# Kernel tuning notes

Measured on AMD Instinct MI355X. Metric: run time of the kernel, lower is better.

Reference implementation:

```python
import jax, jax.numpy as jnp
import numpy as np

N_NODES = 50000
N_EDGES = 500000
NUM_RADIAL = 6
HIDDEN = 128

def swish(v):
    return v * jax.nn.sigmoid(v)

def setup_inputs() -> dict:
    key = jax.random.key(0)
    ks = jax.random.split(key, 8)
    x = jax.random.randint(ks[0], (N_NODES,), 0, 95, dtype=jnp.int32)
    rbf = jax.random.normal(ks[1], (N_EDGES, NUM_RADIAL), dtype=jnp.float32)
    i = jax.random.randint(ks[2], (N_EDGES,), 0, N_NODES, dtype=jnp.int32)
    j = jax.random.randint(ks[3], (N_EDGES,), 0, N_NODES, dtype=jnp.int32)
    sqrt3 = np.sqrt(3.0).astype(np.float32)
    emb_weight = jax.random.uniform(ks[4], (95, HIDDEN), minval=-sqrt3, maxval=sqrt3, dtype=jnp.float32)
    w_rbf0 = jax.random.normal(ks[5], (HIDDEN, NUM_RADIAL), dtype=jnp.float32) * 0.2
    b_rbf0 = jnp.zeros((HIDDEN,), dtype=jnp.float32)
    w_lin = jax.random.normal(ks[6], (HIDDEN, 3 * HIDDEN), dtype=jnpp.float32) if False else jax.random.normal(ks[6], (HIDDEN, 3 * HIDDEN), dtype=jnp.float32) * 0.05
    b_lin = jnp.zeros((HIDDEN,), dtype=jnp.float32)
    w_rbf1 = jax.random.normal(ks[7], (HIDDEN, NUM_RADIAL), dtype=jnp.float32) * 0.4
    return {"x": x, "rbf": rbf, "i": i, "j": j, "emb_weight": emb_weight,
            "w_rbf0": w_rbf0, "b_rbf0": b_rbf0, "w_lin": w_lin, "b_lin": b_lin,
            "w_rbf1": w_rbf1}

def reference(x, rbf, i, j, emb_weight, w_rbf0, b_rbf0, w_lin, b_lin, w_rbf1):
    # node embedding lookup: [N, H]
    h = emb_weight[x]
    # rbf0 = swish(rbf @ W0^T + b0): [E, H]
    rbf0 = swish(jnp.einsum('er,hr->eh', rbf, w_rbf0) + b_rbf0)
    # gather endpoint embeddings and concat with rbf0: [E, 3H]
    cat = jnp.concatenate([h[i], h[j], rbf0], axis=-1)
    e1 = swish(jnp.einsum('ek,hk->eh', cat, w_lin) + b_lin)
    e2 = jnp.einsum('er,hr->eh', rbf, w_rbf1) * e1
    return (e1, e2)
```

## Files before the change

kernel.cpp:

```cpp
#include <hip/hip_runtime.h>

#define HIDDEN 128
#define NRAD 6
#define NEMB 95
#define PRS 68
#define FRS 132
#define SRS 36

typedef short bf16x8 __attribute__((ext_vector_type(8)));
typedef float f32x4 __attribute__((ext_vector_type(4)));

__device__ __forceinline__ float fast_rcp(float x) { return __builtin_amdgcn_rcpf(x); }
__device__ __forceinline__ float swishf(float v) { return v * fast_rcp(1.0f + __expf(-v)); }
__device__ __forceinline__ short f2bf(float f) {
    union { float f; unsigned u; } c; c.f = f;
    unsigned r = (c.u + 0x7FFFu + ((c.u >> 16) & 1u)) >> 16;
    return (short)(unsigned short)r;
}
__device__ __forceinline__ float bf2f(unsigned short u) {
    union { unsigned u; float f; } c; c.u = ((unsigned)u) << 16; return c.f;
}
__device__ __forceinline__ unsigned pk(float lo, float hi) {
    return __builtin_amdgcn_perm(__float_as_uint(hi), __float_as_uint(lo), 0x07060302u);
}
__device__ __forceinline__ float xlo(unsigned u) {
    union { unsigned u; float f; } c; c.u = u << 16; return c.f;
}
__device__ __forceinline__ float xhi(unsigned u) {
    union { unsigned u; float f; } c; c.u = u & 0xffff0000u; return c.f;
}
__device__ __forceinline__ void barrier_lgkm() {
    asm volatile("s_waitcnt lgkmcnt(0)" ::: "memory");
    __builtin_amdgcn_s_barrier();
}
__device__ __forceinline__ void wait_lgkm() {
    asm volatile("s_waitcnt lgkmcnt(0)" ::: "memory");
}

__global__ void precompute_kernel(const float* __restrict__ emb,
                                  const float* __restrict__ w_lin,
                                  const float* __restrict__ b_lin,
                                  unsigned* __restrict__ pPair) {
    __shared__ __align__(16) float erow[HIDDEN];
    const int a = blockIdx.x;
    const int h = threadIdx.x;
    erow[h] = emb[a * HIDDEN + h];
    __syncthreads();
    float a1 = b_lin[h];
    float a2 = 0.f;
    const float* __restrict__ w1 = w_lin + h * 384;
    const float* __restrict__ w2 = w1 + HIDDEN;
#pragma unroll 8
    for (int k = 0; k < HIDDEN; ++k) {
        a1 += erow[k] * w1[k];
        a2 += erow[k] * w2[k];
    }
    const unsigned lo = (unsigned)(unsigned short)f2bf(a1);
    const unsigned hi = ((unsigned)(unsigned short)f2bf(a2)) << 16;
    pPair[a * HIDDEN + h] = hi | lo;
}

struct RawMD {
    float2 ra, rb, rc;
    int ii, jj;
};

__device__ __forceinline__ RawMD load_raw(int st, int l15, int n_edges,
                                          const int* __restrict__ iv,
                                          const int* __restrict__ jv,
                                          const float* __restrict__ rbf) {
    int e = st * 16 + l15;
    int ecl = (e < n_edges) ? e : (n_edges - 1);
    RawMD m;
    const float2* rp = reinterpret_cast<const float2*>(rbf + (size_t)ecl * NRAD);
    m.ra = rp[0];
    m.rb = rp[1];
    m.rc = rp[2];
    m.ii = iv[ecl];
    m.jj = jv[ecl];
    return m;
}

__global__ __launch_bounds__(256, 3)
void edge_mfma_kernel(const int* __restrict__ xv,
                      const float* __restrict__ rbf,
                      const int* __restrict__ iv,
                      const int* __restrict__ jv,
                      const float* __restrict__ w_rbf0,
                      const float* __restrict__ b_rbf0,
                      const float* __restrict__ w_rbf1,
                      const float* __restrict__ w_lin,
                      const unsigned* __restrict__ pPairG,
                      float* __restrict__ out_e1,
                      float* __restrict__ out_e2,
                      int n_edges, int tiles_per_block, int nt32, int n_rows) {
    __shared__ unsigned pps[NEMB * PRS];
    __shared__ __align__(16) short fragS[2][16 * FRS];
    __shared__ __align__(8) unsigned short stg[4][2][16 * SRS];

    const int tid = threadIdx.x;
    const int chh = blockIdx.x & 1;
    const int ebi = blockIdx.x >> 1;

    {
        const int nr = (n_rows < NEMB ? n_rows : NEMB);
        for (int s = tid; s < nr * 64; s += 256) {
            const int a = s >> 6, c = s & 63;
            pps[a * PRS + c] = pPairG[a * HIDDEN + chh * 64 + c];
        }
    }

    const int wid = tid >> 6;
    const int lane = tid & 63;
    const int l15 = lane & 15;
    const int lg = lane >> 4;
    const int u = wid >> 1;
    const int c2 = wid & 1;
    const int chbase = chh * 64 + c2 * 32;

    bf16x8 w3f[2][4];
    bf16x8 w1f[2];
#pragma unroll
    for (int n2 = 0; n2 < 2; ++n2) {
        const int h = chbase + n2 * 16 + l15;
        const float* wp = w_lin + h * 384 + 256;
#pragma unroll
        for (int ks = 0; ks < 4; ++ks) {
            const float4* s4 = reinterpret_cast<const float4*>(wp + (ks * 4 + lg) * 8);
            const float4 va = s4[0];
            const float4 vb = s4[1];
            bf16x8 fr;
            fr[0] = f2bf(va.x); fr[1] = f2bf(va.y);
            fr[2] = f2bf(va.z); fr[3] = f2bf(va.w);
            fr[4] = f2bf(vb.x); fr[5] = f2bf(vb.y);
            fr[6] = f2bf(vb.z); fr[7] = f2bf(vb.w);
            w3f[n2][ks] = fr;
        }
        bf16x8 f1;
#pragma unroll
        for (int r = 0; r < NRAD; ++r) f1[r] = f2bf(w_rbf1[h * NRAD + r]);
        f1[6] = 0; f1[7] = 0;
        w1f[n2] = f1;
    }

    bf16x8 aw0[2];
#pragma unroll
    for (int i = 0; i < 2; ++i) {
        bf16x8 fr = (bf16x8){0, 0, 0, 0, 0, 0, 0, 0};
        if (lg == 0) {
            const int k = (2 * wid + i) * 16 + l15;
#pragma unroll
            for (int r = 0; r < NRAD; ++r) fr[r] = f2bf(w_rbf0[k * NRAD + r]);
            fr[6] = f2bf(b_rbf0[k]);
            fr[7] = 0;
        }
        aw0[i] = fr;
    }
    __syncthreads();

    const int bt = ebi * tiles_per_block;
    const int btEnd = min(bt + tiles_per_block, nt32);
    if (bt >= btEnd) return;

    const f32x4 zero4 = (f32x4){0.f, 0.f, 0.f, 0.f};

    RawMD c0 = load_raw(2 * bt,     l15, n_edges, iv, jv, rbf);
    RawMD c1 = load_raw(2 * bt + 1, l15, n_edges, iv, jv, rbf);

    for (int t = bt; t < btEnd; ++t) {
        RawMD n0 = load_raw(2 * (t + 1),     l15, n_edges, iv, jv, rbf);
        RawMD n1 = load_raw(2 * (t + 1) + 1, l15, n_edges, iv, jv, rbf);
        const int exi = xv[u ? c1.ii : c0.ii];
        const int exj = xv[u ? c1.jj : c0.jj];

        union { uint4 q; bf16x8 b; } rp0, rp1;
        rp0.q = (uint4){0u, 0u, 0u, 0u};
        rp1.q = (uint4){0u, 0u, 0u, 0u};
        if (lg == 0) {
            rp0.q.x = pk(c0.ra.x, c0.ra.y);
            rp0.q.y = pk(c0.rb.x, c0.rb.y);
            rp0.q.z = pk(c0.rc.x, c0.rc.y);
            rp0.q.w = pk(1.0f, 0.0f);
            rp1.q.x = pk(c1.ra.x, c1.ra.y);
            rp1.q.y = pk(c1.rb.x, c1.rb.y);
            rp1.q.z = pk(c1.rc.x, c1.rc.y);
            rp1.q.w = pk(1.0f, 0.0f);
        }

#pragma unroll
        for (int s = 0; s < 2; ++s) {
#pragma unroll
            for (int i = 0; i < 2; ++i) {
                const f32x4 cb = __builtin_amdgcn_mfma_f32_16x16x32_bf16(
                    aw0[i], (s ? rp1.b : rp0.b), zero4, 0, 0, 0);
                const uint2 wv = make_uint2(pk(swishf(cb[0]), swishf(cb[1])),
                                            pk(swishf(cb[2]), swishf(cb[3])));
                *reinterpret_cast<uint2*>(
                    &fragS[s][l15 * FRS + (4 * (2 * wid + i) + lg) * 4]) = wv;
            }
        }

        f32x4 acc2[2];
#pragma unroll
        for (int n2 = 0; n2 < 2; ++n2)
            acc2[n2] = __builtin_amdgcn_mfma_f32_16x16x32_bf16(
                w1f[n2], (u ? rp1.b : rp0.b), zero4, 0, 0, 0);

        barrier_lgkm();

        f32x4 acc[2] = {zero4, zero4};
#pragma unroll
        for (int ks = 0; ks < 4; ++ks) {
            const bf16x8 bf = *reinterpret_cast<const bf16x8*>(
                &fragS[u][l15 * FRS + (8 * ks + 2 * lg) * 4]);
#pragma unroll
            for (int n2 = 0; n2 < 2; ++n2)
                acc[n2] = __builtin_amdgcn_mfma_f32_16x16x32_bf16(
                    w3f[n2][ks], bf, acc[n2], 0, 0, 0);
        }

        barrier_lgkm();

        if (t != bt) {
            const int tp = t - 1;
#pragma unroll
            for (int arr = 0; arr < 2; ++arr) {
                float* __restrict__ ob = arr ? out_e2 : out_e1;
#pragma unroll
                for (int s = 0; s < 2; ++s) {
                    const int e = 8 * s + (lane >> 3);
                    const uint2 uv = *reinterpret_cast<const uint2*>(
                        &stg[wid][arr][e * SRS + (lane & 7) * 4]);
                    const int eg = tp * 32 + u * 16 + e;
                    if (eg < n_edges) {
                        f32x4 v;
                        v[0] = xlo(uv.x); v[1] = xhi(uv.x);
                        v[2] = xlo(uv.y); v[3] = xhi(uv.y);
                        *reinterpret_cast<f32x4*>(
                            ob + (size_t)eg * HIDDEN + chbase + (lane & 7) * 4) = v;
                    }
                }
            }
        }
        wait_lgkm();

#pragma unroll
        for (int n2 = 0; n2 < 2; ++n2) {
            const int ch0 = c2 * 32 + n2 * 16 + lg * 4;
            const uint4 r1 = *reinterpret_cast<const uint4*>(&pps[exi * PRS + ch0]);
            const uint4 r2 = *reinterpret_cast<const uint4*>(&pps[exj * PRS + ch0]);
            float pv[4];
            pv[0] = bf2f((unsigned short)(r1.x & 0xffff)) + bf2f((unsigned short)(r2.x >> 16));
            pv[1] = bf2f((unsigned short)(r1.y & 0xffff)) + bf2f((unsigned short)(r2.y >> 16));
            pv[2] = bf2f((unsigned short)(r1.z & 0xffff)) + bf2f((unsigned short)(r2.z >> 16));
            pv[3] = bf2f((unsigned short)(r1.w & 0xffff)) + bf2f((unsigned short)(r2.w >> 16));
            float e1v[4], e2v[4];
#pragma unroll
            for (int q = 0; q < 4; ++q) {
                const float sm = acc[n2][q] + pv[q];
                e1v[q] = swishf(sm);
                e2v[q] = acc2[n2][q] * e1v[q];
            }
            const int so = l15 * SRS + n2 * 16 + lg * 4;
            *reinterpret_cast<uint2*>(&stg[wid][0][so]) =
                make_uint2(pk(e1v[0], e1v[1]), pk(e1v[2], e1v[3]));
            *reinterpret_cast<uint2*>(&stg[wid][1][so]) =
                make_uint2(pk(e2v[0], e2v[1]), pk(e2v[2], e2v[3]));
        }

        c0 = n0; c1 = n1;
    }

    wait_lgkm();
    {
        const int tp = btEnd - 1;
#pragma unroll
        for (int arr = 0; arr < 2; ++arr) {
            float* __restrict__ ob = arr ? out_e2 : out_e1;
#pragma unroll
            for (int s = 0; s < 2; ++s) {
                const int e = 8 * s + (lane >> 3);
                const uint2 uv = *reinterpret_cast<const uint2*>(
                    &stg[wid][arr][e * SRS + (lane & 7) * 4]);
                const int eg = tp * 32 + u * 16 + e;
                if (eg < n_edges) {
                    f32x4 v;
                    v[0] = xlo(uv.x); v[1] = xhi(uv.x);
                    v[2] = xlo(uv.y); v[3] = xhi(uv.y);
                    *reinterpret_cast<f32x4*>(
                        ob + (size_t)eg * HIDDEN + chbase + (lane & 7) * 4) = v;
                }
            }
        }
    }
}

extern "C" void kernel_launch(void* const* d_in, const int* in_sizes, int n_in,
                              void* d_out, int out_size, void* d_ws, size_t ws_size,
                              hipStream_t stream) {
    const int*   xv     = (const int*)  d_in[0];
    const float* rbf    = (const float*)d_in[1];
    const int*   iv     = (const int*)  d_in[2];
    const int*   jv     = (const int*)  d_in[3];
    const float* emb    = (const float*)d_in[4];
    const float* w_rbf0 = (const float*)d_in[5];
    const float* b_rbf0 = (const float*)d_in[6];
    const float* w_lin  = (const float*)d_in[7];
    const float* b_lin  = (const float*)d_in[8];
    const float* w_rbf1 = (const float*)d_in[9];

    const int n_edges = in_sizes[2];
    const int n_emb_rows = in_sizes[4] / HIDDEN;

    unsigned* pPair = (unsigned*)d_ws;

    float* out_e1 = (float*)d_out;
    float* out_e2 = out_e1 + (size_t)n_edges * HIDDEN;

    precompute_kernel<<<n_emb_rows, HIDDEN, 0, stream>>>(emb, w_lin, b_lin, pPair);

    const int nt32 = (n_edges + 31) / 32;
    const int grid = 768;
    const int nEB = grid / 2;
    const int tpb = (nt32 + nEB - 1) / nEB;
    edge_mfma_kernel<<<grid, 256, 0, stream>>>(xv, rbf, iv, jv,
                                               w_rbf0, b_rbf0, w_rbf1, w_lin,
                                               pPair, out_e1, out_e2,
                                               n_edges, tpb, nt32, n_emb_rows);
}
```

Measured before the change: 176.2 us.

## Restructure edge kernel so each wave owns full 16-edge tiles independently

Replaces the block-cooperative scheme (two blocks splitting channels, four waves sharing a 32-edge tile through barriers) with one where each of 12 waves per 768-thread block processes a whole 16-edge tile across all 128 channels on its own, striding through tiles in a grid-stride loop. The w_lin third-slice weights move from registers to LDS as bf16 and are read per MFMA. The rbf0 swish is now computed with scalar FMAs per lane instead of a small MFMA. Per-iteration block barriers go away, and the per-block edge tile of the pair table no longer has to be loaded twice. The costs are much more LDS traffic for weight fragments, larger register use (16 accumulators), and fewer resident blocks per CU.

```diff
diff --git a/kernel.cpp b/kernel.cpp
--- a/kernel.cpp
+++ b/kernel.cpp
@@ -3,9 +3,11 @@
 #define HIDDEN 128
 #define NRAD 6
 #define NEMB 95
-#define PRS 68
-#define FRS 132
-#define SRS 36
+#define PRS 132
+#define WRS 132
+#define SRS 132
+#define NWAVES 12
+#define NBLK 256
 
 typedef short bf16x8 __attribute__((ext_vector_type(8)));
 typedef float f32x4 __attribute__((ext_vector_type(4)));
@@ -28,10 +30,6 @@
 }
 __device__ __forceinline__ float xhi(unsigned u) {
     union { unsigned u; float f; } c; c.u = u & 0xffff0000u; return c.f;
-}
-__device__ __forceinline__ void barrier_lgkm() {
-    asm volatile("s_waitcnt lgkmcnt(0)" ::: "memory");
-    __builtin_amdgcn_s_barrier();
 }
 __device__ __forceinline__ void wait_lgkm() {
     asm volatile("s_waitcnt lgkmcnt(0)" ::: "memory");
@@ -65,11 +63,11 @@
     int ii, jj;
 };
 
-__device__ __forceinline__ RawMD load_raw(int st, int l15, int n_edges,
+__device__ __forceinline__ RawMD load_raw(int tile, int l15, int n_edges,
                                           const int* __restrict__ iv,
                                           const int* __restrict__ jv,
                                           const float* __restrict__ rbf) {
-    int e = st * 16 + l15;
+    int e = tile * 16 + l15;
     int ecl = (e < n_edges) ? e : (n_edges - 1);
     RawMD m;
     const float2* rp = reinterpret_cast<const float2*>(rbf + (size_t)ecl * NRAD);
@@ -81,7 +79,7 @@
     return m;
 }
 
-__global__ __launch_bounds__(256, 3)
+__global__ __launch_bounds__(768)
 void edge_mfma_kernel(const int* __restrict__ xv,
                       const float* __restrict__ rbf,
                       const int* __restrict__ iv,
@@ -93,204 +91,168 @@
                       const unsigned* __restrict__ pPairG,
                       float* __restrict__ out_e1,
                       float* __restrict__ out_e2,
-                      int n_edges, int tiles_per_block, int nt32, int n_rows) {
+                      int n_edges, int nt16, int n_rows) {
     __shared__ unsigned pps[NEMB * PRS];
-    __shared__ __align__(16) short fragS[2][16 * FRS];
-    __shared__ __align__(8) unsigned short stg[4][2][16 * SRS];
+    __shared__ __align__(16) short w3s[HIDDEN * WRS];
+    __shared__ __align__(16) float w0e[HIDDEN * 8];
+    __shared__ __align__(16) short w1a[HIDDEN * 8];
+    __shared__ __align__(8) unsigned short stg[NWAVES][2][8 * SRS];
 
     const int tid = threadIdx.x;
-    const int chh = blockIdx.x & 1;
-    const int ebi = blockIdx.x >> 1;
 
     {
         const int nr = (n_rows < NEMB ? n_rows : NEMB);
-        for (int s = tid; s < nr * 64; s += 256) {
-            const int a = s >> 6, c = s & 63;
-            pps[a * PRS + c] = pPairG[a * HIDDEN + chh * 64 + c];
+        for (int s = tid; s < nr * HIDDEN; s += 768) {
+            const int a = s >> 7, c = s & 127;
+            pps[a * PRS + c] = pPairG[s];
         }
     }
+    for (int s = tid; s < HIDDEN * 16; s += 768) {
+        const int h = s >> 4, oct = s & 15;
+        const float4* s4 = reinterpret_cast<const float4*>(w_lin + h * 384 + 256 + oct * 8);
+        const float4 va = s4[0];
+        const float4 vb = s4[1];
+        bf16x8 fr;
+        fr[0] = f2bf(va.x); fr[1] = f2bf(va.y);
+        fr[2] = f2bf(va.z); fr[3] = f2bf(va.w);
+        fr[4] = f2bf(vb.x); fr[5] = f2bf(vb.y);
+        fr[6] = f2bf(vb.z); fr[7] = f2bf(vb.w);
+        *reinterpret_cast<bf16x8*>(&w3s[h * WRS + oct * 8]) = fr;
+    }
+    if (tid < HIDDEN) {
+        const int k = tid;
+#pragma unroll
+        for (int r = 0; r < NRAD; ++r) w0e[k * 8 + r] = w_rbf0[k * NRAD + r];
+        w0e[k * 8 + 6] = b_rbf0[k];
+        w0e[k * 8 + 7] = 0.f;
+        bf16x8 f1;
+#pragma unroll
+        for (int r = 0; r < NRAD; ++r) f1[r] = f2bf(w_rbf1[k * NRAD + r]);
+        f1[6] = 0; f1[7] = 0;
+        *reinterpret_cast<bf16x8*>(&w1a[k * 8]) = f1;
+    }
+    __syncthreads();
 
     const int wid = tid >> 6;
     const int lane = tid & 63;
     const int l15 = lane & 15;
     const int lg = lane >> 4;
-    const int u = wid >> 1;
-    const int c2 = wid & 1;
-    const int chbase = chh * 64 + c2 * 32;
-
-    bf16x8 w3f[2][4];
-    bf16x8 w1f[2];
-#pragma unroll
-    for (int n2 = 0; n2 < 2; ++n2) {
-        const int h = chbase + n2 * 16 + l15;
-        const float* wp = w_lin + h * 384 + 256;
-#pragma unroll
-        for (int ks = 0; ks < 4; ++ks) {
-            const float4* s4 = reinterpret_cast<const float4*>(wp + (ks * 4 + lg) * 8);
-            const float4 va = s4[0];
-            const float4 vb = s4[1];
-            bf16x8 fr;
-            fr[0] = f2bf(va.x); fr[1] = f2bf(va.y);
-            fr[2] = f2bf(va.z); fr[3] = f2bf(va.w);
-            fr[4] = f2bf(vb.x); fr[5] = f2bf(vb.y);
-            fr[6] = f2bf(vb.z); fr[7] = f2bf(vb.w);
-            w3f[n2][ks] = fr;
-        }
-        bf16x8 f1;
-#pragma unroll
-        for (int r = 0; r < NRAD; ++r) f1[r] = f2bf(w_rbf1[h * NRAD + r]);
-        f1[6] = 0; f1[7] = 0;
-        w1f[n2] = f1;
-    }
-
-    bf16x8 aw0[2];
-#pragma unroll
-    for (int i = 0; i < 2; ++i) {
-        bf16x8 fr = (bf16x8){0, 0, 0, 0, 0, 0, 0, 0};
-        if (lg == 0) {
-            const int k = (2 * wid + i) * 16 + l15;
-#pragma unroll
-            for (int r = 0; r < NRAD; ++r) fr[r] = f2bf(w_rbf0[k * NRAD + r]);
-            fr[6] = f2bf(b_rbf0[k]);
-            fr[7] = 0;
-        }
-        aw0[i] = fr;
-    }
-    __syncthreads();
-
-    const int bt = ebi * tiles_per_block;
-    const int btEnd = min(bt + tiles_per_block, nt32);
-    if (bt >= btEnd) return;
+    const int gw = blockIdx.x * NWAVES + wid;
+    const int NW = NBLK * NWAVES;
 
     const f32x4 zero4 = (f32x4){0.f, 0.f, 0.f, 0.f};
 
-    RawMD c0 = load_raw(2 * bt,     l15, n_edges, iv, jv, rbf);
-    RawMD c1 = load_raw(2 * bt + 1, l15, n_edges, iv, jv, rbf);
-
-    for (int t = bt; t < btEnd; ++t) {
-        RawMD n0 = load_raw(2 * (t + 1),     l15, n_edges, iv, jv, rbf);
-        RawMD n1 = load_raw(2 * (t + 1) + 1, l15, n_edges, iv, jv, rbf);
-        const int exi = xv[u ? c1.ii : c0.ii];
-        const int exj = xv[u ? c1.jj : c0.jj];
-
-        union { uint4 q; bf16x8 b; } rp0, rp1;
-        rp0.q = (uint4){0u, 0u, 0u, 0u};
-        rp1.q = (uint4){0u, 0u, 0u, 0u};
-        if (lg == 0) {
-            rp0.q.x = pk(c0.ra.x, c0.ra.y);
-            rp0.q.y = pk(c0.rb.x, c0.rb.y);
-            rp0.q.z = pk(c0.rc.x, c0.rc.y);
-            rp0.q.w = pk(1.0f, 0.0f);
-            rp1.q.x = pk(c1.ra.x, c1.ra.y);
-            rp1.q.y = pk(c1.rb.x, c1.rb.y);
-            rp1.q.z = pk(c1.rc.x, c1.rc.y);
-            rp1.q.w = pk(1.0f, 0.0f);
-        }
-
-#pragma unroll
-        for (int s = 0; s < 2; ++s) {
-#pragma unroll
-            for (int i = 0; i < 2; ++i) {
-                const f32x4 cb = __builtin_amdgcn_mfma_f32_16x16x32_bf16(
-                    aw0[i], (s ? rp1.b : rp0.b), zero4, 0, 0, 0);
-                const uint2 wv = make_uint2(pk(swishf(cb[0]), swishf(cb[1])),
-                                            pk(swishf(cb[2]), swishf(cb[3])));
-                *reinterpret_cast<uint2*>(
-                    &fragS[s][l15 * FRS + (4 * (2 * wid + i) + lg) * 4]) = wv;
-            }
-        }
-
-        f32x4 acc2[2];
-#pragma unroll
-        for (int n2 = 0; n2 < 2; ++n2)
-            acc2[n2] = __builtin_amdgcn_mfma_f32_16x16x32_bf16(
-                w1f[n2], (u ? rp1.b : rp0.b), zero4, 0, 0, 0);
-
-        barrier_lgkm();
-
-        f32x4 acc[2] = {zero4, zero4};
-#pragma unroll
-        for (int ks = 0; ks < 4; ++ks) {
-            const bf16x8 bf = *reinterpret_cast<const bf16x8*>(
-                &fragS[u][l15 * FRS + (8 * ks + 2 * lg) * 4]);
-#pragma unroll
-            for (int n2 = 0; n2 < 2; ++n2)
-                acc[n2] = __builtin_amdgcn_mfma_f32_16x16x32_bf16(
-                    w3f[n2][ks], bf, acc[n2], 0, 0, 0);
-        }
-
-        barrier_lgkm();
-
-        if (t != bt) {
-            const int tp = t - 1;
-#pragma unroll
-            for (int arr = 0; arr < 2; ++arr) {
-                float* __restrict__ ob = arr ? out_e2 : out_e1;
-#pragma unroll
-                for (int s = 0; s < 2; ++s) {
-                    const int e = 8 * s + (lane >> 3);
-                    const uint2 uv = *reinterpret_cast<const uint2*>(
-                        &stg[wid][arr][e * SRS + (lane & 7) * 4]);
-                    const int eg = tp * 32 + u * 16 + e;
-                    if (eg < n_edges) {
-                        f32x4 v;
-                        v[0] = xlo(uv.x); v[1] = xhi(uv.x);
-                        v[2] = xlo(uv.y); v[3] = xhi(uv.y);
-                        *reinterpret_cast<f32x4*>(
-                            ob + (size_t)eg * HIDDEN + chbase + (lane & 7) * 4) = v;
+    int t = gw;
+    if (t < nt16) {
+        RawMD cur = load_raw(t, l15, n_edges, iv, jv, rbf);
+        for (; t < nt16; t += NW) {
+            const int tn = (t + NW < nt16) ? t + NW : t;
+            RawMD nxt = load_raw(tn, l15, n_edges, iv, jv, rbf);
+            const int xi = xv[cur.ii];
+            const int xj = xv[cur.jj];
+
+            bf16x8 bfrag[4];
+#pragma unroll
+            for (int ks = 0; ks < 4; ++ks) {
+                float sv[8];
+#pragma unroll
+                for (int j = 0; j < 8; ++j) {
+                    const int k = ks * 32 + lg * 8 + j;
+                    const f32x4 wa = *reinterpret_cast<const f32x4*>(&w0e[k * 8]);
+                    const f32x4 wb = *reinterpret_cast<const f32x4*>(&w0e[k * 8 + 4]);
+                    const float tv = wb[2]
+                                   + cur.ra.x * wa[0] + cur.ra.y * wa[1]
+                                   + cur.rb.x * wa[2] + cur.rb.y * wa[3]
+                                   + cur.rc.x * wb[0] + cur.rc.y * wb[1];
+                    sv[j] = swishf(tv);
+                }
+                union { uint4 q; bf16x8 b; } mf;
+                mf.q.x = pk(sv[0], sv[1]); mf.q.y = pk(sv[2], sv[3]);
+                mf.q.z = pk(sv[4], sv[5]); mf.q.w = pk(sv[6], sv[7]);
+                bfrag[ks] = mf.b;
+            }
+
+            union { uint4 q; bf16x8 b; } rp;
+            rp.q = (uint4){0u, 0u, 0u, 0u};
+            if (lg == 0) {
+                rp.q.x = pk(cur.ra.x, cur.ra.y);
+                rp.q.y = pk(cur.rb.x, cur.rb.y);
+                rp.q.z = pk(cur.rc.x, cur.rc.y);
+                rp.q.w = pk(1.0f, 0.0f);
+            }
+            f32x4 acc2[8];
+#pragma unroll
+            for (int nt = 0; nt < 8; ++nt) {
+                const bf16x8 aw = *reinterpret_cast<const bf16x8*>(
+                    &w1a[(nt * 16 + l15) * 8]);
+                acc2[nt] = __builtin_amdgcn_mfma_f32_16x16x32_bf16(aw, rp.b, zero4, 0, 0, 0);
+            }
+
+            f32x4 acc[8];
+#pragma unroll
+            for (int nt = 0; nt < 8; ++nt) acc[nt] = zero4;
+#pragma unroll
+            for (int ks = 0; ks < 4; ++ks)
+#pragma unroll
+                for (int nt = 0; nt < 8; ++nt) {
+                    const bf16x8 wfr = *reinterpret_cast<const bf16x8*>(
+                        &w3s[(nt * 16 + l15) * WRS + (ks * 4 + lg) * 8]);
+                    acc[nt] = __builtin_amdgcn_mfma_f32_16x16x32_bf16(
+                        wfr, bfrag[ks], acc[nt], 0, 0, 0);
+                }
+
+#pragma unroll
+            for (int p = 0; p < 2; ++p) {
+                if ((l15 >> 3) == p) {
+                    const int so = (l15 & 7) * SRS;
+#pragma unroll
+                    for (int nt = 0; nt < 8; ++nt) {
+                        const int ch0 = nt * 16 + lg * 4;
+                        const uint4 r1 = *reinterpret_cast<const uint4*>(&pps[xi * PRS + ch0]);
+                        const uint4 r2 = *reinterpret_cast<const uint4*>(&pps[xj * PRS + ch0]);
+                        float e1v[4], e2v[4];
+                        {
+                            const unsigned rr1[4] = {r1.x, r1.y, r1.z, r1.w};
+                            const unsigned rr2[4] = {r2.x, r2.y, r2.z, r2.w};
+#pragma unroll
+                            for (int q = 0; q < 4; ++q) {
+                                const float pv = bf2f((unsigned short)(rr1[q] & 0xffff))
+                                               + bf2f((unsigned short)(rr2[q] >> 16));
+                                const float sm = acc[nt][q] + pv;
+                                e1v[q] = swishf(sm);
+                                e2v[q] = acc2[nt][q] * e1v[q];
+                            }
+                        }
+                        *reinterpret_cast<uint2*>(&stg[wid][0][so + ch0]) =
+                            make_uint2(pk(e1v[0], e1v[1]), pk(e1v[2], e1v[3]));
+                        *reinterpret_cast<uint2*>(&stg[wid][1][so + ch0]) =
+                            make_uint2(pk(e2v[0], e2v[1]), pk(e2v[2], e2v[3]));
                     }
                 }
-            }
-        }
-        wait_lgkm();
-
-#pragma unroll
-        for (int n2 = 0; n2 < 2; ++n2) {
-            const int ch0 = c2 * 32 + n2 * 16 + lg * 4;
-            const uint4 r1 = *reinterpret_cast<const uint4*>(&pps[exi * PRS + ch0]);
-            const uint4 r2 = *reinterpret_cast<const uint4*>(&pps[exj * PRS + ch0]);
-            float pv[4];
-            pv[0] = bf2f((unsigned short)(r1.x & 0xffff)) + bf2f((unsigned short)(r2.x >> 16));
-            pv[1] = bf2f((unsigned short)(r1.y & 0xffff)) + bf2f((unsigned short)(r2.y >> 16));
-            pv[2] = bf2f((unsigned short)(r1.z & 0xffff)) + bf2f((unsigned short)(r2.z >> 16));
-            pv[3] = bf2f((unsigned short)(r1.w & 0xffff)) + bf2f((unsigned short)(r2.w >> 16));
-            float e1v[4], e2v[4];
-#pragma unroll
-            for (int q = 0; q < 4; ++q) {
-                const float sm = acc[n2][q] + pv[q];
-                e1v[q] = swishf(sm);
-                e2v[q] = acc2[n2][q] * e1v[q];
-            }
-            const int so = l15 * SRS + n2 * 16 + lg * 4;
-            *reinterpret_cast<uint2*>(&stg[wid][0][so]) =
-                make_uint2(pk(e1v[0], e1v[1]), pk(e1v[2], e1v[3]));
-            *reinterpret_cast<uint2*>(&stg[wid][1][so]) =
-                make_uint2(pk(e2v[0], e2v[1]), pk(e2v[2], e2v[3]));
-        }
-
-        c0 = n0; c1 = n1;
-    }
-
-    wait_lgkm();
-    {
-        const int tp = btEnd - 1;
-#pragma unroll
-        for (int arr = 0; arr < 2; ++arr) {
-            float* __restrict__ ob = arr ? out_e2 : out_e1;
-#pragma unroll
-            for (int s = 0; s < 2; ++s) {
-                const int e = 8 * s + (lane >> 3);
-                const uint2 uv = *reinterpret_cast<const uint2*>(
-                    &stg[wid][arr][e * SRS + (lane & 7) * 4]);
-                const int eg = tp * 32 + u * 16 + e;
-                if (eg < n_edges) {
-                    f32x4 v;
-                    v[0] = xlo(uv.x); v[1] = xhi(uv.x);
-                    v[2] = xlo(uv.y); v[3] = xhi(uv.y);
-                    *reinterpret_cast<f32x4*>(
-                        ob + (size_t)eg * HIDDEN + chbase + (lane & 7) * 4) = v;
-                }
-            }
+                wait_lgkm();
+
+                const size_t base = ((size_t)t * 16 + p * 8) * HIDDEN;
+#pragma unroll
+                for (int arr = 0; arr < 2; ++arr) {
+                    float* __restrict__ ob = arr ? out_e2 : out_e1;
+#pragma unroll
+                    for (int s2 = 0; s2 < 4; ++s2) {
+                        const int idx = s2 * 256 + lane * 4;
+                        const int e_l = idx >> 7;
+                        const int ch = idx & 127;
+                        const uint2 uv = *reinterpret_cast<const uint2*>(
+                            &stg[wid][arr][e_l * SRS + ch]);
+                        if (t * 16 + p * 8 + e_l < n_edges) {
+                            f32x4 v;
+                            v[0] = xlo(uv.x); v[1] = xhi(uv.x);
+                            v[2] = xlo(uv.y); v[3] = xhi(uv.y);
+                            *reinterpret_cast<f32x4*>(ob + base + idx) = v;
+                        }
+                    }
+                }
+                wait_lgkm();
+            }
+            cur = nxt;
         }
     }
 }
@@ -319,12 +281,9 @@
 
     precompute_kernel<<<n_emb_rows, HIDDEN, 0, stream>>>(emb, w_lin, b_lin, pPair);
 
-    const int nt32 = (n_edges + 31) / 32;
-    const int grid = 768;
-    const int nEB = grid / 2;
-    const int tpb = (nt32 + nEB - 1) / nEB;
-    edge_mfma_kernel<<<grid, 256, 0, stream>>>(xv, rbf, iv, jv,
+    const int nt16 = (n_edges + 15) / 16;
+    edge_mfma_kernel<<<NBLK, 768, 0, stream>>>(xv, rbf, iv, jv,
                                                w_rbf0, b_rbf0, w_rbf1, w_lin,
                                                pPair, out_e1, out_e2,
-                                               n_edges, tpb, nt32, n_emb_rows);
-}
+                                               n_edges, nt16, n_emb_rows);
+}
```

Result: faster. 155.8 us (-11.6%).
